# Performance work log

Measured on AMD Instinct MI355X. Metric: run time of the kernel, lower is better.

## Reference

```python
import jax, jax.numpy as jnp
import numpy as np

N = 20000      # nodes
E = 320000     # edges (avg degree 16)
D = 256        # embedding_dim
H = 8          # num_heads
DH = D // H    # head_dim = 32
ED = 64        # edge_dim
FF = 4 * D     # feed-forward hidden
EPS = 1e-5


def setup_inputs() -> dict:
    key = jax.random.key(0)
    ks = jax.random.split(key, 32)

    def lin_w(k, i, o):
        return (jax.random.normal(k, (i, o), jnp.float32) / np.sqrt(i)).astype(jnp.float32)

    return {
        "x": jax.random.normal(ks[0], (N, D), jnp.float32),
        "edge_features": jax.random.normal(ks[1], (E, ED), jnp.float32),
        "edge_weights": jax.random.uniform(ks[2], (E,), jnp.float32),
        "edge_index": jax.random.randint(ks[3], (2, E), 0, N, dtype=jnp.int32),
        "Wq": lin_w(ks[4], D, D), "bq": jnp.zeros((D,), jnp.float32),
        "Wk": lin_w(ks[5], D, D), "bk": jnp.zeros((D,), jnp.float32),
        "Wv": lin_w(ks[6], D, D), "bv": jnp.zeros((D,), jnp.float32),
        "We": lin_w(ks[7], ED, DH), "be": jnp.zeros((DH,), jnp.float32),
        "Wo": lin_w(ks[8], D, D), "bo": jnp.zeros((D,), jnp.float32),
        "ln1_g": jnp.ones((D,), jnp.float32), "ln1_b": jnp.zeros((D,), jnp.float32),
        "ln2_g": jnp.ones((D,), jnp.float32), "ln2_b": jnp.zeros((D,), jnp.float32),
        "W1": lin_w(ks[9], D, FF), "b1": jnp.zeros((FF,), jnp.float32),
        "W2": lin_w(ks[10], FF, D), "b2": jnp.zeros((D,), jnp.float32),
        "alpha": jnp.ones((1,), jnp.float32),
        "beta": jnp.ones((1,), jnp.float32),
    }


def _layernorm(x, g, b):
    m = jnp.mean(x, axis=-1, keepdims=True)
    v = jnp.var(x, axis=-1, keepdims=True)
    return (x - m) * jax.lax.rsqrt(v + EPS) * g + b


def _edge_attention(xn, edge_index, ef, ew, Wq, bq, Wk, bk, Wv, bv, We, be, Wo, bo):
    n = xn.shape[0]
    scale = DH ** -0.5
    q = (xn @ Wq + bq).reshape(n, H, DH)
    k = (xn @ Wk + bk).reshape(n, H, DH)
    v = (xn @ Wv + bv).reshape(n, H, DH)
    src, dst = edge_index[0], edge_index[1]
    ep = ef @ We + be                               # [E, DH], shared across heads
    # per-edge, per-head scores: q[dst] . (k[src] + edge_proj)
    scores = jnp.einsum('ehd,ehd->eh', q[dst], k[src] + ep[:, None, :]) * scale
    scores = scores * ew[:, None]
    # segment softmax over incoming edges of each dst node
    m = jax.ops.segment_max(scores, dst, num_segments=n)
    m = jnp.where(jnp.isfinite(m), m, 0.0)          # nodes with no incoming edges
    ex = jnp.exp(scores - m[dst])
    s = jax.ops.segment_sum(ex, dst, num_segments=n)
    attn = ex / s[dst]                              # [E, H]
    # scatter-weighted V aggregation; nodes with no edges stay zero (matches torch)
    out = jax.ops.segment_sum(attn[:, :, None] * v[src], dst, num_segments=n)
    out = out.reshape(n, D) @ Wo + bo
    return out


def reference(x, edge_features, edge_weights, edge_index,
              Wq, bq, Wk, bk, Wv, bv, We, be, Wo, bo,
              ln1_g, ln1_b, ln2_g, ln2_b, W1, b1, W2, b2, alpha, beta):
    xn = _layernorm(x, ln1_g, ln1_b)
    attn_out = _edge_attention(xn, edge_index, edge_features, edge_weights,
                               Wq, bq, Wk, bk, Wv, bv, We, be, Wo, bo)
    x = x + alpha * attn_out
    xn = _layernorm(x, ln2_g, ln2_b)
    ff = jax.nn.gelu(xn @ W1 + b1, approximate=False) @ W2 + b2
    x = x + beta * ff
    return x
```

## Files before the change

kernel.cpp:

```cpp
#include <hip/hip_runtime.h>
#include <math.h>

#define NN 20000
#define EE 320000
#define DD 256
#define HH 8
#define DHD 32
#define EDF 64
#define FFD 1024

typedef unsigned short u16;
typedef __attribute__((ext_vector_type(8))) __bf16 bf16x8;
typedef __attribute__((ext_vector_type(8))) unsigned short u16x8;
typedef __attribute__((ext_vector_type(4))) float f32x4;

#define XN_OFF   (0)
#define AGGB_OFF (2560000)
#define X1_OFF   (5120000)
#define QKV_OFF  (10240000)
#define EP_OFF   (25600000)
#define WT_OFF   (35840000)
#define BQKV_OFF (36240000)
#define CSR_OFF  (36250000)

__device__ __forceinline__ u16 f2bf(float f) {
    unsigned u = __float_as_uint(f);
    return (u16)((u + 0x7FFFu + ((u >> 16) & 1u)) >> 16);
}
__device__ __forceinline__ float bf2f(u16 h) {
    return __uint_as_float(((unsigned)h) << 16);
}
__device__ __forceinline__ float gelu_exact(float v) {
    return 0.5f * v * (1.0f + erff(v * 0.70710678118654752f));
}

#define GLDS16(g, l) __builtin_amdgcn_global_load_lds(             \
    (__attribute__((address_space(1))) void*)(g),                  \
    (__attribute__((address_space(3))) void*)(l), 16, 0, 0)

__device__ __forceinline__ void ln_body(const float* __restrict__ x,
                                        const float* __restrict__ g,
                                        const float* __restrict__ b,
                                        u16* __restrict__ out, int vb) {
    int row = vb * 4 + (threadIdx.x >> 6);
    if (row >= NN) return;
    int lane = threadIdx.x & 63;
    float4 v = *(const float4*)&x[(size_t)row * DD + lane * 4];
    float s  = v.x + v.y + v.z + v.w;
    float ss = v.x * v.x + v.y * v.y + v.z * v.z + v.w * v.w;
    #pragma unroll
    for (int o = 32; o >= 1; o >>= 1) {
        s  += __shfl_xor(s, o);
        ss += __shfl_xor(ss, o);
    }
    float mean = s * (1.0f / DD);
    float var  = ss * (1.0f / DD) - mean * mean;
    float inv  = rsqrtf(var + 1e-5f);
    float4 gg = *(const float4*)&g[lane * 4];
    float4 bb = *(const float4*)&b[lane * 4];
    ushort4 o4;
    o4.x = f2bf((v.x - mean) * inv * gg.x + bb.x);
    o4.y = f2bf((v.y - mean) * inv * gg.y + bb.y);
    o4.z = f2bf((v.z - mean) * inv * gg.z + bb.z);
    o4.w = f2bf((v.w - mean) * inv * gg.w + bb.w);
    *(ushort4*)&out[(size_t)row * DD + lane * 4] = o4;
}

__global__ __launch_bounds__(256) void ln_kernel(const float* __restrict__ x,
                                                 const float* __restrict__ g,
                                                 const float* __restrict__ b,
                                                 u16* __restrict__ out) {
    ln_body(x, g, b, out, blockIdx.x);
}

__device__ __forceinline__ void transp_body(const float* __restrict__ src,
                                            u16* __restrict__ dst,
                                            int K, int N, int k0, int n0) {
    __shared__ float Ws[64][65];
    int t = threadIdx.x;
    int rr = t >> 4, cc = (t & 15) * 4;
    if (n0 + cc < N) {
        #pragma unroll
        for (int p = 0; p < 4; p++) {
            int k = rr + p * 16;
            float4 v = *(const float4*)&src[(size_t)(k0 + k) * N + n0 + cc];
            Ws[k][cc + 0] = v.x; Ws[k][cc + 1] = v.y;
            Ws[k][cc + 2] = v.z; Ws[k][cc + 3] = v.w;
        }
    }
    __syncthreads();
    int n = t >> 2, kc = (t & 3) * 16;
    if (n0 + n < N) {
        u16 o[16];
        #pragma unroll
        for (int j = 0; j < 16; j++) o[j] = f2bf(Ws[kc + j][n]);
        u16* dp = dst + (size_t)(n0 + n) * K + k0 + kc;
        *(ushort4*)(dp + 0)  = *(ushort4*)&o[0];
        *(ushort4*)(dp + 4)  = *(ushort4*)&o[4];
        *(ushort4*)(dp + 8)  = *(ushort4*)&o[8];
        *(ushort4*)(dp + 12) = *(ushort4*)&o[12];
    }
}

__global__ __launch_bounds__(256) void prep_count_ln_kernel(
    const float* __restrict__ Wq, const float* __restrict__ Wk,
    const float* __restrict__ Wv, const float* __restrict__ Wo,
    const float* __restrict__ W1, const float* __restrict__ W2,
    const float* __restrict__ We,
    const float* __restrict__ bq, const float* __restrict__ bk,
    const float* __restrict__ bv,
    u16* __restrict__ WqkvT, u16* __restrict__ WoT, u16* __restrict__ W1T,
    u16* __restrict__ W2T, u16* __restrict__ WeT, float* __restrict__ bqkv,
    const int* __restrict__ ei, int* __restrict__ counts,
    const float* __restrict__ x, const float* __restrict__ ln1g,
    const float* __restrict__ ln1b, u16* __restrict__ xn) {
    int b = blockIdx.x;
    if (b < 193) {
        const float* src; u16* dst; int K, N, ti;
        if      (b < 16)  { src = Wq; dst = WqkvT;          K = 256;  N = 256;  ti = b; }
        else if (b < 32)  { src = Wk; dst = WqkvT + 65536;  K = 256;  N = 256;  ti = b - 16; }
        else if (b < 48)  { src = Wv; dst = WqkvT + 131072; K = 256;  N = 256;  ti = b - 32; }
        else if (b < 64)  { src = Wo; dst = WoT;            K = 256;  N = 256;  ti = b - 48; }
        else if (b < 128) { src = W1; dst = W1T;            K = 256;  N = 1024; ti = b - 64; }
        else if (b < 192) { src = W2; dst = W2T;            K = 1024; N = 256;  ti = b - 128; }
        else              { src = We; dst = WeT;            K = 64;   N = 32;   ti = 0; }
        int ntn = N >> 6; if (ntn == 0) ntn = 1;
        int tk = ti / ntn, tn = ti % ntn;
        transp_body(src, dst, K, N, tk * 64, tn * 64);
    } else if (b == 193) {
        int t = threadIdx.x;
        bqkv[t] = bq[t];
        bqkv[256 + t] = bk[t];
        bqkv[512 + t] = bv[t];
    } else if (b < 1444) {
        int e = (b - 194) * 256 + threadIdx.x;
        if (e < EE) atomicAdd(&counts[ei[EE + e]], 1);
    } else {
        ln_body(x, ln1g, ln1b, xn, b - 1444);
    }
}

template <int BM, int BN, int EPI>
__device__ __forceinline__ void gemm_body(
    char* smem,
    const u16* __restrict__ A, const u16* __restrict__ BT,
    const float* __restrict__ bias,
    float* __restrict__ Cf, u16* __restrict__ Cb,
    const float* __restrict__ res, const float* __restrict__ scale,
    int M, int K, int N, int bxx, int byy)
{
    constexpr int FM = BM / 32, FN = BN / 32;
    constexpr int nA = BM / 32, nB = BN / 32;
    constexpr int NST = (nA > nB) ? nA : nB;
    u16* Asm = (u16*)smem;
    u16* Bsm = (u16*)(smem + BM * 64 * 2);
    const int tid  = threadIdx.x;
    const int lane = tid & 63;
    const int w    = tid >> 6;
    const int wr   = w >> 1, wc = w & 1;
    const int bm   = bxx * BM;
    const int bn   = byy * BN;

    f32x4 acc[FM][FN] = {};

    int st_row[NST], st_src[NST], st_dst[NST];
    #pragma unroll
    for (int i = 0; i < NST; i++) {
        int base  = i * 4096 + w * 1024;
        int off   = base + lane * 16;
        int row   = off >> 7;
        int inner = off & 127;
        st_row[i] = row;
        st_src[i] = (inner ^ ((row & 7) << 4)) >> 1;
        st_dst[i] = base;
    }
    const int arow0 = wr * (BM / 2) + (lane & 15);
    const int brow0 = wc * (BN / 2) + (lane & 15);
    const int kb0   = (lane >> 4) * 16;

    for (int k0 = 0; k0 < K; k0 += 64) {
        #pragma unroll
        for (int i = 0; i < nA; i++) {
            int r = bm + st_row[i]; if (r > M - 1) r = M - 1;
            GLDS16(A + (size_t)r * K + k0 + st_src[i], (char*)Asm + st_dst[i]);
        }
        #pragma unroll
        for (int i = 0; i < nB; i++) {
            int r = bn + st_row[i];
            GLDS16(BT + (size_t)r * K + k0 + st_src[i], (char*)Bsm + st_dst[i]);
        }
        asm volatile("s_waitcnt vmcnt(0)" ::: "memory");
        __syncthreads();
        #pragma unroll
        for (int s = 0; s < 2; s++) {
            bf16x8 af[FM], bfv[FN];
            #pragma unroll
            for (int i = 0; i < FM; i++) {
                int row  = arow0 + i * 16;
                int byte = (row << 7) + ((kb0 + s * 64) ^ ((row & 7) << 4));
                af[i] = *(const bf16x8*)((const char*)Asm + byte);
            }
            #pragma unroll
            for (int j = 0; j < FN; j++) {
                int row  = brow0 + j * 16;
                int byte = (row << 7) + ((kb0 + s * 64) ^ ((row & 7) << 4));
                bfv[j] = *(const bf16x8*)((const char*)Bsm + byte);
            }
            #pragma unroll
            for (int i = 0; i < FM; i++)
                #pragma unroll
                for (int j = 0; j < FN; j++)
                    acc[i][j] = __builtin_amdgcn_mfma_f32_16x16x32_bf16(
                        af[i], bfv[j], acc[i][j], 0, 0, 0);
        }
        __syncthreads();
    }

    float sc = 0.f;
    if constexpr (EPI == 2) sc = scale[0];
    const int col0 = bn + wc * (BN / 2) + (lane & 15);
    const int row0 = bm + wr * (BM / 2) + ((lane >> 4) << 2);
    #pragma unroll
    for (int i = 0; i < FM; i++) {
        #pragma unroll
        for (int j = 0; j < FN; j++) {
            int col = col0 + j * 16;
            float bb = bias[col];
            #pragma unroll
            for (int r = 0; r < 4; r++) {
                int row = row0 + i * 16 + r;
                if (row < M) {
                    float o = acc[i][j][r] + bb;
                    if constexpr (EPI == 1) {
                        Cb[(size_t)row * N + col] = f2bf(gelu_exact(o));
                    } else if constexpr (EPI == 2) {
                        Cf[(size_t)row * N + col] = res[(size_t)row * N + col] + sc * o;
                    } else if constexpr (EPI == 3) {
                        if (col < 256) {
                            Cb[(size_t)row * 256 + col] = f2bf(o * 0.17677669529663689f);
                        } else if (col < 512) {
                            Cb[(size_t)NN * 256 + (size_t)row * 512 + (col - 256) * 2] = f2bf(o);
                        } else {
                            Cb[(size_t)NN * 256 + (size_t)row * 512 + (col - 512) * 2 + 1] = f2bf(o);
                        }
                    } else {
                        Cf[(size_t)row * N + col] = o;
                    }
                }
            }
        }
    }
}

template <int BM, int BN, int EPI>
__global__ __launch_bounds__(256) void gemm_bf16(
    const u16* __restrict__ A, const u16* __restrict__ BT,
    const float* __restrict__ bias,
    float* __restrict__ Cf, u16* __restrict__ Cb,
    const float* __restrict__ res, const float* __restrict__ scale,
    int M, int K, int N) {
    __shared__ char smem[(BM + BN) * 64 * 2];
    gemm_body<BM, BN, EPI>(smem, A, BT, bias, Cf, Cb, res, scale, M, K, N,
                           blockIdx.x, blockIdx.y);
}

__device__ __forceinline__ void ep_body(char* smem,
                                        const float* __restrict__ ef,
                                        const u16* __restrict__ WeT,
                                        const float* __restrict__ be,
                                        const int* __restrict__ epos,
                                        u16* __restrict__ epc, int blk) {
    const int tid  = threadIdx.x;
    const int lane = tid & 63;
    const int w    = tid >> 6;
    const int e0b  = blk * 64;

    #pragma unroll
    for (int j = 0; j < 4; j++) {
        int gidx = (w * 4 + j) * 64 + lane;
        int e    = gidx >> 4;
        int cs   = (gidx & 15) << 4;
        int c    = cs ^ ((e & 15) << 4);
        GLDS16((const char*)ef + (size_t)(e0b + e) * 256 + c,
               smem + (w * 4 + j) * 1024);
    }
    asm volatile("s_waitcnt vmcnt(0)" ::: "memory");
    __syncthreads();

    const int ar = lane & 15;
    const int r  = w * 16 + ar;
    const int e0 = e0b + w * 16;

    f32x4 acc[2] = {};
    #pragma unroll
    for (int s = 0; s < 2; s++) {
        int cbyte = (lane >> 4) * 32 + s * 128;
        const char* base = smem + r * 256;
        float4 a0 = *(const float4*)(base + ((cbyte)      ^ (ar << 4)));
        float4 a1 = *(const float4*)(base + ((cbyte + 16) ^ (ar << 4)));
        bf16x8 af;
        af[0] = (__bf16)a0.x; af[1] = (__bf16)a0.y; af[2] = (__bf16)a0.z; af[3] = (__bf16)a0.w;
        af[4] = (__bf16)a1.x; af[5] = (__bf16)a1.y; af[6] = (__bf16)a1.z; af[7] = (__bf16)a1.w;
        #pragma unroll
        for (int j = 0; j < 2; j++) {
            bf16x8 bf = *(const bf16x8*)&WeT[(size_t)(j * 16 + ar) * EDF + s * 32 + ((lane >> 4) * 8)];
            acc[j] = __builtin_amdgcn_mfma_f32_16x16x32_bf16(af, bf, acc[j], 0, 0, 0);
        }
    }
    const int row0 = (lane >> 4) << 2;
    #pragma unroll
    for (int rr = 0; rr < 4; rr++) {
        int pos = epos[e0 + row0 + rr];
        #pragma unroll
        for (int j = 0; j < 2; j++) {
            int col = j * 16 + ar;
            epc[(size_t)pos * DHD + col] = f2bf(acc[j][rr] + be[col]);
        }
    }
}

__global__ __launch_bounds__(256) void qkv_ep_kernel(
    const u16* __restrict__ xn, const u16* __restrict__ WqkvT,
    const float* __restrict__ bqkv, u16* __restrict__ qb,
    const float* __restrict__ ef, const u16* __restrict__ WeT,
    const float* __restrict__ be, const int* __restrict__ epos,
    u16* __restrict__ epc) {
    __shared__ char smem[32768];
    int b = blockIdx.x;
    if (b < 942) {
        gemm_body<128, 128, 3>(smem, xn, WqkvT, bqkv, nullptr, qb, nullptr,
                               nullptr, NN, DD, 768, b % 157, b / 157);
    } else {
        ep_body(smem, ef, WeT, be, epos, epc, b - 942);
    }
}

__global__ __launch_bounds__(1024) void scan_kernel(const int* __restrict__ counts,
                                                    int* __restrict__ row_start,
                                                    int* __restrict__ cursor) {
    __shared__ int part[1024];
    const int CH = 20;
    int t = threadIdx.x;
    int base = t * CH;
    int loc[CH];
    int s = 0;
    #pragma unroll
    for (int i = 0; i < CH; i++) {
        int idx = base + i;
        int c = (idx < NN) ? counts[idx] : 0;
        loc[i] = s;
        s += c;
    }
    part[t] = s;
    __syncthreads();
    for (int o = 1; o < 1024; o <<= 1) {
        int vv = (t >= o) ? part[t - o] : 0;
        __syncthreads();
        part[t] += vv;
        __syncthreads();
    }
    int off = (t > 0) ? part[t - 1] : 0;
    #pragma unroll
    for (int i = 0; i < CH; i++) {
        int idx = base + i;
        if (idx < NN) {
            int rs = off + loc[i];
            row_start[idx] = rs;
            cursor[idx] = rs;
        }
    }
    if (t == 1023) row_start[NN] = part[1023];
}

__global__ __launch_bounds__(256) void fill_kernel(const int* __restrict__ ei,
                                                   const float* __restrict__ ew,
                                                   int* __restrict__ cursor,
                                                   int2* __restrict__ csr,
                                                   int* __restrict__ epos) {
    int e = blockIdx.x * 256 + threadIdx.x;
    if (e >= EE) return;
    int src = ei[e];
    int dst = ei[EE + e];
    int pos = atomicAdd(&cursor[dst], 1);
    csr[pos] = make_int2(src, __float_as_int(ew[e] * 1.44269504088896f));
    epos[e] = pos;
}

__global__ __launch_bounds__(256) void attn_kernel(const u16* __restrict__ qb,
                                                   const u16* __restrict__ kv,
                                                   const u16* __restrict__ epc,
                                                   const int2* __restrict__ csr,
                                                   const int* __restrict__ row_start,
                                                   u16* __restrict__ aggb) {
    const int dst  = blockIdx.x * 4 + (threadIdx.x >> 6);
    const int lane = threadIdx.x & 63;
    const int g    = lane & 7;
    const int d0   = (lane >> 3) * 32 + g * 4;
    const int beg = row_start[dst];
    const int end = row_start[dst + 1];
    ushort4 q4 = *(const ushort4*)&qb[(size_t)dst * DD + d0];
    float4 qv = make_float4(bf2f(q4.x), bf2f(q4.y), bf2f(q4.z), bf2f(q4.w));
    float ss = 0.f;
    float4 acc = make_float4(0.f, 0.f, 0.f, 0.f);

    int i = beg;
    if ((i & 1) && i < end) {
        int2 p = csr[i];
        u16x8 kk = *(const u16x8*)&kv[(size_t)p.x * 512 + d0 * 2];
        ushort4 e4 = *(const ushort4*)&epc[(size_t)i * DHD + g * 4];
        float k0 = bf2f(kk[0]) + bf2f(e4.x);
        float k1 = bf2f(kk[2]) + bf2f(e4.y);
        float k2 = bf2f(kk[4]) + bf2f(e4.z);
        float k3 = bf2f(kk[6]) + bf2f(e4.w);
        float pv = fmaf(qv.x, k0, fmaf(qv.y, k1, fmaf(qv.z, k2, qv.w * k3)));
        #pragma unroll
        for (int o = 4; o >= 1; o >>= 1) pv += __shfl_xor(pv, o);
        float wq = exp2f(pv * __int_as_float(p.y));
        ss += wq;
        acc.x = fmaf(wq, bf2f(kk[1]), acc.x);
        acc.y = fmaf(wq, bf2f(kk[3]), acc.y);
        acc.z = fmaf(wq, bf2f(kk[5]), acc.z);
        acc.w = fmaf(wq, bf2f(kk[7]), acc.w);
        ++i;
    }
    for (; i + 4 <= end; i += 4) {
        int4 c01 = *(const int4*)&csr[i];
        int4 c23 = *(const int4*)&csr[i + 2];
        int   sr[4] = {c01.x, c01.z, c23.x, c23.z};
        float wt[4] = {__int_as_float(c01.y), __int_as_float(c01.w),
                       __int_as_float(c23.y), __int_as_float(c23.w)};
        u16x8 kk[4];
        ushort4 e4[4];
        #pragma unroll
        for (int u = 0; u < 4; u++) {
            kk[u] = *(const u16x8*)&kv[(size_t)sr[u] * 512 + d0 * 2];
            e4[u] = *(const ushort4*)&epc[(size_t)(i + u) * DHD + g * 4];
        }
        float pp[4];
        #pragma unroll
        for (int u = 0; u < 4; u++) {
            float k0 = bf2f(kk[u][0]) + bf2f(e4[u].x);
            float k1 = bf2f(kk[u][2]) + bf2f(e4[u].y);
            float k2 = bf2f(kk[u][4]) + bf2f(e4[u].z);
            float k3 = bf2f(kk[u][6]) + bf2f(e4[u].w);
            pp[u] = fmaf(qv.x, k0, fmaf(qv.y, k1, fmaf(qv.z, k2, qv.w * k3)));
        }
        #pragma unroll
        for (int o = 4; o >= 1; o >>= 1) {
            #pragma unroll
            for (int u = 0; u < 4; u++) pp[u] += __shfl_xor(pp[u], o);
        }
        #pragma unroll
        for (int u = 0; u < 4; u++) {
            float wq = exp2f(pp[u] * wt[u]);
            ss += wq;
            acc.x = fmaf(wq, bf2f(kk[u][1]), acc.x);
            acc.y = fmaf(wq, bf2f(kk[u][3]), acc.y);
            acc.z = fmaf(wq, bf2f(kk[u][5]), acc.z);
            acc.w = fmaf(wq, bf2f(kk[u][7]), acc.w);
        }
    }
    for (; i < end; ++i) {
        int2 p = csr[i];
        u16x8 kk = *(const u16x8*)&kv[(size_t)p.x * 512 + d0 * 2];
        ushort4 e4 = *(const ushort4*)&epc[(size_t)i * DHD + g * 4];
        float k0 = bf2f(kk[0]) + bf2f(e4.x);
        float k1 = bf2f(kk[2]) + bf2f(e4.y);
        float k2 = bf2f(kk[4]) + bf2f(e4.z);
        float k3 = bf2f(kk[6]) + bf2f(e4.w);
        float pv = fmaf(qv.x, k0, fmaf(qv.y, k1, fmaf(qv.z, k2, qv.w * k3)));
        #pragma unroll
        for (int o = 4; o >= 1; o >>= 1) pv += __shfl_xor(pv, o);
        float wq = exp2f(pv * __int_as_float(p.y));
        ss += wq;
        acc.x = fmaf(wq, bf2f(kk[1]), acc.x);
        acc.y = fmaf(wq, bf2f(kk[3]), acc.y);
        acc.z = fmaf(wq, bf2f(kk[5]), acc.z);
        acc.w = fmaf(wq, bf2f(kk[7]), acc.w);
    }
    float inv = (end > beg) ? 1.f / ss : 0.f;
    ushort4 o4;
    o4.x = f2bf(acc.x * inv);
    o4.y = f2bf(acc.y * inv);
    o4.z = f2bf(acc.z * inv);
    o4.w = f2bf(acc.w * inv);
    *(ushort4*)&aggb[(size_t)dst * DD + d0] = o4;
}

extern "C" void kernel_launch(void* const* d_in, const int* in_sizes, int n_in,
                              void* d_out, int out_size, void* d_ws, size_t ws_size,
                              hipStream_t stream) {
    const float* x    = (const float*)d_in[0];
    const float* ef   = (const float*)d_in[1];
    const float* ew   = (const float*)d_in[2];
    const int*   ei   = (const int*)d_in[3];
    const float* Wq   = (const float*)d_in[4];
    const float* bq   = (const float*)d_in[5];
    const float* Wk   = (const float*)d_in[6];
    const float* bk   = (const float*)d_in[7];
    const float* Wv   = (const float*)d_in[8];
    const float* bv   = (const float*)d_in[9];
    const float* We   = (const float*)d_in[10];
    const float* be   = (const float*)d_in[11];
    const float* Wo   = (const float*)d_in[12];
    const float* bo   = (const float*)d_in[13];
    const float* ln1g = (const float*)d_in[14];
    const float* ln1b = (const float*)d_in[15];
    const float* ln2g = (const float*)d_in[16];
    const float* ln2b = (const float*)d_in[17];
    const float* W1   = (const float*)d_in[18];
    const float* b1   = (const float*)d_in[19];
    const float* W2   = (const float*)d_in[20];
    const float* b2   = (const float*)d_in[21];
    const float* alpha = (const float*)d_in[22];
    const float* beta  = (const float*)d_in[23];

    float* ws    = (float*)d_ws;
    u16*   xn    = (u16*)(ws + XN_OFF);
    u16*   aggb  = (u16*)(ws + AGGB_OFF);
    float* x1    = ws + X1_OFF;
    u16*   qb    = (u16*)(ws + QKV_OFF);
    u16*   kv    = qb + (size_t)NN * 256;
    u16*   ff1   = (u16*)(ws + QKV_OFF);
    u16*   epc   = (u16*)(ws + EP_OFF);
    u16*   wt    = (u16*)(ws + WT_OFF);
    u16*   WqkvT = wt;
    u16*   WoT   = wt + 768 * 256;
    u16*   W1T   = WoT + 256 * 256;
    u16*   W2T   = W1T + 1024 * 256;
    u16*   WeT   = W2T + 256 * 1024;
    float* bqkv  = ws + BQKV_OFF;
    float* out   = (float*)d_out;

    int*  counts    = (int*)(ws + CSR_OFF);
    int*  row_start = counts + NN;
    int*  cursor    = row_start + NN + 1;
    int2* csr       = (int2*)(counts + 60004);
    int*  epos      = counts + 60004 + 2 * EE;

    hipMemsetAsync(counts, 0, (size_t)NN * sizeof(int), stream);

    prep_count_ln_kernel<<<6444, 256, 0, stream>>>(
        Wq, Wk, Wv, Wo, W1, W2, We, bq, bk, bv,
        WqkvT, WoT, W1T, W2T, WeT, bqkv, ei, counts, x, ln1g, ln1b, xn);

    scan_kernel<<<1, 1024, 0, stream>>>(counts, row_start, cursor);
    fill_kernel<<<EE / 256, 256, 0, stream>>>(ei, ew, cursor, csr, epos);

    qkv_ep_kernel<<<5942, 256, 0, stream>>>(xn, WqkvT, bqkv, qb,
                                            ef, WeT, be, epos, epc);

    attn_kernel<<<NN / 4, 256, 0, stream>>>(qb, kv, epc, csr, row_start, aggb);

    gemm_bf16<64, 128, 2><<<dim3(313, 2), 256, 0, stream>>>(
        aggb, WoT, bo, x1, nullptr, x, alpha, NN, DD, DD);

    ln_kernel<<<NN / 4, 256, 0, stream>>>(x1, ln2g, ln2b, xn);

    gemm_bf16<128, 128, 1><<<dim3(157, 8), 256, 0, stream>>>(
        xn, W1T, b1, nullptr, ff1, nullptr, nullptr, NN, DD, FFD);
    gemm_bf16<64, 128, 2><<<dim3(313, 2), 256, 0, stream>>>(
        ff1, W2T, b2, out, nullptr, x1, beta, NN, FFD, DD);
}
```

Baseline: 263.9 us.

## Schedule attention by descending in-degree and gather edge features in CSR order

Nodes are bucketed by in-degree (capped at 63) in the scan kernel, and the fill kernel writes a degree-descending node order that the attention kernel uses to pick which destination each wave processes. This is meant to balance load so heavy nodes start first and waves in a block have similar edge counts. The edge-projection pass now gathers edge_features rows by CSR position through an edge-id array and writes epc contiguously, replacing scattered 2-byte stores with gathered 256-byte reads. The cost is an extra indirection in the ep loads and the attention node index, plus a few atomics.

```diff
diff --git a/kernel.cpp b/kernel.cpp
--- a/kernel.cpp
+++ b/kernel.cpp
@@ -268,20 +268,21 @@
                                         const float* __restrict__ ef,
                                         const u16* __restrict__ WeT,
                                         const float* __restrict__ be,
-                                        const int* __restrict__ epos,
+                                        const int* __restrict__ eids,
                                         u16* __restrict__ epc, int blk) {
     const int tid  = threadIdx.x;
     const int lane = tid & 63;
     const int w    = tid >> 6;
-    const int e0b  = blk * 64;
+    const int p0   = blk * 64;
 
     #pragma unroll
     for (int j = 0; j < 4; j++) {
         int gidx = (w * 4 + j) * 64 + lane;
-        int e    = gidx >> 4;
+        int row  = gidx >> 4;
         int cs   = (gidx & 15) << 4;
-        int c    = cs ^ ((e & 15) << 4);
-        GLDS16((const char*)ef + (size_t)(e0b + e) * 256 + c,
+        int c    = cs ^ ((row & 15) << 4);
+        int e    = eids[p0 + row];
+        GLDS16((const char*)ef + (size_t)e * 256 + c,
                smem + (w * 4 + j) * 1024);
     }
     asm volatile("s_waitcnt vmcnt(0)" ::: "memory");
@@ -289,7 +290,6 @@
 
     const int ar = lane & 15;
     const int r  = w * 16 + ar;
-    const int e0 = e0b + w * 16;
 
     f32x4 acc[2] = {};
     #pragma unroll
@@ -310,7 +310,7 @@
     const int row0 = (lane >> 4) << 2;
     #pragma unroll
     for (int rr = 0; rr < 4; rr++) {
-        int pos = epos[e0 + row0 + rr];
+        int pos = p0 + w * 16 + row0 + rr;
         #pragma unroll
         for (int j = 0; j < 2; j++) {
             int col = j * 16 + ar;
@@ -323,7 +323,7 @@
     const u16* __restrict__ xn, const u16* __restrict__ WqkvT,
     const float* __restrict__ bqkv, u16* __restrict__ qb,
     const float* __restrict__ ef, const u16* __restrict__ WeT,
-    const float* __restrict__ be, const int* __restrict__ epos,
+    const float* __restrict__ be, const int* __restrict__ eids,
     u16* __restrict__ epc) {
     __shared__ char smem[32768];
     int b = blockIdx.x;
@@ -331,16 +331,20 @@
         gemm_body<128, 128, 3>(smem, xn, WqkvT, bqkv, nullptr, qb, nullptr,
                                nullptr, NN, DD, 768, b % 157, b / 157);
     } else {
-        ep_body(smem, ef, WeT, be, epos, epc, b - 942);
+        ep_body(smem, ef, WeT, be, eids, epc, b - 942);
     }
 }
 
 __global__ __launch_bounds__(1024) void scan_kernel(const int* __restrict__ counts,
                                                     int* __restrict__ row_start,
-                                                    int* __restrict__ cursor) {
+                                                    int* __restrict__ cursor,
+                                                    int* __restrict__ dcursor) {
     __shared__ int part[1024];
+    __shared__ int hist[64];
     const int CH = 20;
     int t = threadIdx.x;
+    if (t < 64) hist[t] = 0;
+    __syncthreads();
     int base = t * CH;
     int loc[CH];
     int s = 0;
@@ -348,6 +352,7 @@
     for (int i = 0; i < CH; i++) {
         int idx = base + i;
         int c = (idx < NN) ? counts[idx] : 0;
+        if (idx < NN) atomicAdd(&hist[min(c, 63)], 1);
         loc[i] = s;
         s += c;
     }
@@ -370,20 +375,36 @@
         }
     }
     if (t == 1023) row_start[NN] = part[1023];
+    if (t < 64) {
+        int st = 0;
+        for (int b = 63; b > t; --b) st += hist[b];
+        dcursor[t] = st;
+    }
 }
 
 __global__ __launch_bounds__(256) void fill_kernel(const int* __restrict__ ei,
                                                    const float* __restrict__ ew,
                                                    int* __restrict__ cursor,
                                                    int2* __restrict__ csr,
-                                                   int* __restrict__ epos) {
-    int e = blockIdx.x * 256 + threadIdx.x;
-    if (e >= EE) return;
-    int src = ei[e];
-    int dst = ei[EE + e];
-    int pos = atomicAdd(&cursor[dst], 1);
-    csr[pos] = make_int2(src, __float_as_int(ew[e] * 1.44269504088896f));
-    epos[e] = pos;
+                                                   int* __restrict__ eids,
+                                                   const int* __restrict__ counts,
+                                                   int* __restrict__ dcursor,
+                                                   int* __restrict__ order) {
+    int b = blockIdx.x;
+    if (b < EE / 256) {
+        int e = b * 256 + threadIdx.x;
+        int src = ei[e];
+        int dst = ei[EE + e];
+        int pos = atomicAdd(&cursor[dst], 1);
+        csr[pos] = make_int2(src, __float_as_int(ew[e] * 1.44269504088896f));
+        eids[pos] = e;
+    } else {
+        int n = (b - EE / 256) * 256 + threadIdx.x;
+        if (n < NN) {
+            int pos = atomicAdd(&dcursor[min(counts[n], 63)], 1);
+            order[pos] = n;
+        }
+    }
 }
 
 __global__ __launch_bounds__(256) void attn_kernel(const u16* __restrict__ qb,
@@ -391,8 +412,9 @@
                                                    const u16* __restrict__ epc,
                                                    const int2* __restrict__ csr,
                                                    const int* __restrict__ row_start,
+                                                   const int* __restrict__ order,
                                                    u16* __restrict__ aggb) {
-    const int dst  = blockIdx.x * 4 + (threadIdx.x >> 6);
+    const int dst  = order[blockIdx.x * 4 + (threadIdx.x >> 6)];
     const int lane = threadIdx.x & 63;
     const int g    = lane & 7;
     const int d0   = (lane >> 3) * 32 + g * 4;
@@ -536,7 +558,9 @@
     int*  row_start = counts + NN;
     int*  cursor    = row_start + NN + 1;
     int2* csr       = (int2*)(counts + 60004);
-    int*  epos      = counts + 60004 + 2 * EE;
+    int*  eids      = counts + 60004 + 2 * EE;
+    int*  order     = eids + EE;
+    int*  dcursor   = order + NN;
 
     hipMemsetAsync(counts, 0, (size_t)NN * sizeof(int), stream);
 
@@ -544,13 +568,14 @@
         Wq, Wk, Wv, Wo, W1, W2, We, bq, bk, bv,
         WqkvT, WoT, W1T, W2T, WeT, bqkv, ei, counts, x, ln1g, ln1b, xn);
 
-    scan_kernel<<<1, 1024, 0, stream>>>(counts, row_start, cursor);
-    fill_kernel<<<EE / 256, 256, 0, stream>>>(ei, ew, cursor, csr, epos);
+    scan_kernel<<<1, 1024, 0, stream>>>(counts, row_start, cursor, dcursor);
+    fill_kernel<<<EE / 256 + (NN + 255) / 256, 256, 0, stream>>>(
+        ei, ew, cursor, csr, eids, counts, dcursor, order);
 
     qkv_ep_kernel<<<5942, 256, 0, stream>>>(xn, WqkvT, bqkv, qb,
-                                            ef, WeT, be, epos, epc);
-
-    attn_kernel<<<NN / 4, 256, 0, stream>>>(qb, kv, epc, csr, row_start, aggb);
+                                            ef, WeT, be, eids, epc);
+
+    attn_kernel<<<NN / 4, 256, 0, stream>>>(qb, kv, epc, csr, row_start, order, aggb);
 
     gemm_bf16<64, 128, 2><<<dim3(313, 2), 256, 0, stream>>>(
         aggb, WoT, bo, x1, nullptr, x, alpha, NN, DD, DD);
```

New measurement: 310.8 us. +17.8%, slower.

## Schedule attention wavefronts by descending in-degree to balance load

Applied to the files above, without the earlier changes.

Builds a degree histogram in the scan kernel and, inside the fill kernel, a counting-sort permutation of destination nodes ordered by descending in-degree (capped at 63). The attention kernel then reads each wavefront's destination from this order, so high-degree nodes start first and the four nodes sharing a block have similar edge counts. This is meant to cut the tail imbalance and idle lanes that random degree variation causes. It costs extra atomics in the scan and fill kernels, an indirect load in the attention kernel, and less locality in the q and output row accesses.

```diff
diff --git a/kernel.cpp b/kernel.cpp
--- a/kernel.cpp
+++ b/kernel.cpp
@@ -337,17 +337,26 @@
 
 __global__ __launch_bounds__(1024) void scan_kernel(const int* __restrict__ counts,
                                                     int* __restrict__ row_start,
-                                                    int* __restrict__ cursor) {
+                                                    int* __restrict__ cursor,
+                                                    int* __restrict__ dcursor) {
     __shared__ int part[1024];
+    __shared__ int hist[64][16];
     const int CH = 20;
     int t = threadIdx.x;
+    if (t < 64) {
+        #pragma unroll
+        for (int s = 0; s < 16; s++) hist[t][s] = 0;
+    }
+    __syncthreads();
     int base = t * CH;
+    int sub = t & 15;
     int loc[CH];
     int s = 0;
     #pragma unroll
     for (int i = 0; i < CH; i++) {
         int idx = base + i;
         int c = (idx < NN) ? counts[idx] : 0;
+        if (idx < NN) atomicAdd(&hist[min(c, 63)][sub], 1);
         loc[i] = s;
         s += c;
     }
@@ -370,20 +379,49 @@
         }
     }
     if (t == 1023) row_start[NN] = part[1023];
+    if (t < 64) {
+        int st = 0;
+        for (int b = 63; b > t; --b) {
+            #pragma unroll
+            for (int sj = 0; sj < 16; sj++) st += hist[b][sj];
+        }
+        dcursor[t] = st;
+    }
 }
 
 __global__ __launch_bounds__(256) void fill_kernel(const int* __restrict__ ei,
                                                    const float* __restrict__ ew,
                                                    int* __restrict__ cursor,
                                                    int2* __restrict__ csr,
-                                                   int* __restrict__ epos) {
-    int e = blockIdx.x * 256 + threadIdx.x;
-    if (e >= EE) return;
-    int src = ei[e];
-    int dst = ei[EE + e];
-    int pos = atomicAdd(&cursor[dst], 1);
-    csr[pos] = make_int2(src, __float_as_int(ew[e] * 1.44269504088896f));
-    epos[e] = pos;
+                                                   int* __restrict__ epos,
+                                                   const int* __restrict__ counts,
+                                                   int* __restrict__ dcursor,
+                                                   int* __restrict__ order) {
+    int b = blockIdx.x;
+    if (b < EE / 256) {
+        int e = b * 256 + threadIdx.x;
+        int src = ei[e];
+        int dst = ei[EE + e];
+        int pos = atomicAdd(&cursor[dst], 1);
+        csr[pos] = make_int2(src, __float_as_int(ew[e] * 1.44269504088896f));
+        epos[e] = pos;
+    } else {
+        __shared__ int lhist[64];
+        __shared__ int lbase[64];
+        int t = threadIdx.x;
+        if (t < 64) lhist[t] = 0;
+        __syncthreads();
+        int n = (b - EE / 256) * 256 + t;
+        int d = -1, lpos = 0;
+        if (n < NN) {
+            d = min(counts[n], 63);
+            lpos = atomicAdd(&lhist[d], 1);
+        }
+        __syncthreads();
+        if (t < 64 && lhist[t] > 0) lbase[t] = atomicAdd(&dcursor[t], lhist[t]);
+        __syncthreads();
+        if (n < NN) order[lbase[d] + lpos] = n;
+    }
 }
 
 __global__ __launch_bounds__(256) void attn_kernel(const u16* __restrict__ qb,
@@ -391,8 +429,9 @@
                                                    const u16* __restrict__ epc,
                                                    const int2* __restrict__ csr,
                                                    const int* __restrict__ row_start,
+                                                   const int* __restrict__ order,
                                                    u16* __restrict__ aggb) {
-    const int dst  = blockIdx.x * 4 + (threadIdx.x >> 6);
+    const int dst  = order[blockIdx.x * 4 + (threadIdx.x >> 6)];
     const int lane = threadIdx.x & 63;
     const int g    = lane & 7;
     const int d0   = (lane >> 3) * 32 + g * 4;
@@ -537,6 +576,8 @@
     int*  cursor    = row_start + NN + 1;
     int2* csr       = (int2*)(counts + 60004);
     int*  epos      = counts + 60004 + 2 * EE;
+    int*  order     = epos + EE;
+    int*  dcursor   = order + NN;
 
     hipMemsetAsync(counts, 0, (size_t)NN * sizeof(int), stream);
 
@@ -544,13 +585,14 @@
         Wq, Wk, Wv, Wo, W1, W2, We, bq, bk, bv,
         WqkvT, WoT, W1T, W2T, WeT, bqkv, ei, counts, x, ln1g, ln1b, xn);
 
-    scan_kernel<<<1, 1024, 0, stream>>>(counts, row_start, cursor);
-    fill_kernel<<<EE / 256, 256, 0, stream>>>(ei, ew, cursor, csr, epos);
+    scan_kernel<<<1, 1024, 0, stream>>>(counts, row_start, cursor, dcursor);
+    fill_kernel<<<EE / 256 + (NN + 255) / 256, 256, 0, stream>>>(
+        ei, ew, cursor, csr, epos, counts, dcursor, order);
 
     qkv_ep_kernel<<<5942, 256, 0, stream>>>(xn, WqkvT, bqkv, qb,
                                             ef, WeT, be, epos, epc);
 
-    attn_kernel<<<NN / 4, 256, 0, stream>>>(qb, kv, epc, csr, row_start, aggb);
+    attn_kernel<<<NN / 4, 256, 0, stream>>>(qb, kv, epc, csr, row_start, order, aggb);
 
     gemm_bf16<64, 128, 2><<<dim3(313, 2), 256, 0, stream>>>(
         aggb, WoT, bo, x1, nullptr, x, alpha, NN, DD, DD);
```

Result: no change. 264.2 us (+0.1%).
